# Kernel optimization log

Hardware: AMD Instinct MI355X
Metric: run time of the kernel (lower is better)

The kernel has to match this reference:

```python
import jax, jax.numpy as jnp
import numpy as np

NEG_SLOPE = 0.01  # LeakyReLU default


def gcn_conv(x, src, dst, W, b, num_nodes):
    """PyG GCNConv: x' = D^-1/2 (A+I) D^-1/2 (x W) + b, self-loops added."""
    h = x @ W
    loop = jnp.arange(num_nodes)
    s = jnp.concatenate([src, loop])
    d = jnp.concatenate([dst, loop])
    deg = jax.ops.segment_sum(jnp.ones(s.shape[0], dtype=h.dtype), d,
                              num_segments=num_nodes)
    dinv = jnp.where(deg > 0, jax.lax.rsqrt(deg), 0.0)
    norm = dinv[s] * dinv[d]              # (Ep+N,)
    out = jax.ops.segment_sum(h[s] * norm[:, None], d, num_segments=num_nodes)
    return out + b


def leaky_relu(x):
    return jnp.where(x > 0, x, NEG_SLOPE * x)


def setup_inputs() -> dict:
    key = jax.random.key(0)
    ks = jax.random.split(key, 8)
    B, V, E, Fsub, H = 16, 100000, 300000, 800000, 16
    verts = jax.random.normal(ks[0], (B, V, 3), dtype=jnp.float32)
    edges = jax.random.randint(ks[1], (E, 2), 0, V)
    faces_sub = jax.random.randint(ks[2], (Fsub, 3), 0, V + E)
    W1 = jax.random.normal(ks[3], (3, H), dtype=jnp.float32) * 0.01
    W2 = jax.random.normal(ks[4], (H, H), dtype=jnp.float32) * 0.01
    W3 = jax.random.normal(ks[5], (H, 3), dtype=jnp.float32) * 0.01
    return {"verts": verts, "edges": edges, "faces_sub": faces_sub,
            "W1": W1, "b1": jnp.zeros((H,), jnp.float32),
            "W2": W2, "b2": jnp.zeros((H,), jnp.float32),
            "W3": W3, "b3": jnp.zeros((3,), jnp.float32)}


def reference(verts, edges, faces_sub, W1, b1, W2, b2, W3, b3):
    B, V, _ = verts.shape
    E = edges.shape[0]
    N = B * V
    # pack edges across the batch (same topology per mesh, offset per mesh)
    offsets = (jnp.arange(B) * V).astype(edges.dtype)
    pe = (edges[None, :, :] + offsets[:, None, None]).reshape(B * E, 2)
    src, dst = pe[:, 0], pe[:, 1]

    x = verts.reshape(N, 3)
    h = leaky_relu(gcn_conv(x, src, dst, W1, b1, N))
    h = leaky_relu(gcn_conv(h, src, dst, W2, b2, N))
    # Dropout(0.5) is identity at inference
    offs = gcn_conv(h, src, dst, W3, b3, N)

    v = (x + offs).reshape(B, V, 3)          # offset_verts
    mid = v[:, edges].mean(axis=2)           # (B, E, 3) edge midpoints
    new_verts = jnp.concatenate([v, mid], axis=1)   # (B, V+E, 3)
    new_faces = jnp.broadcast_to(faces_sub[None], (B,) + faces_sub.shape)
    return new_verts, new_faces
```

## Files before the change

kernel.cpp:

```cpp
#include <hip/hip_runtime.h>
#include <hip/hip_bf16.h>

#define NEG_SLOPE 0.01f

typedef long long i64;
typedef __hip_bfloat16 bf16;

__device__ __forceinline__ float lrelu(float x) { return x > 0.f ? x : NEG_SLOPE * x; }
__device__ __forceinline__ float b2f(bf16 v) { return __bfloat162float(v); }
__device__ __forceinline__ float lo2f(unsigned u) { return __uint_as_float(u << 16); }
__device__ __forceinline__ float hi2f(unsigned u) { return __uint_as_float(u & 0xffff0000u); }
__device__ __forceinline__ unsigned pk2(float a, float b) {
    unsigned ua = __bfloat16_as_ushort(__float2bfloat16(a));
    unsigned ub = __bfloat16_as_ushort(__float2bfloat16(b));
    return ua | (ub << 16);
}
__device__ __forceinline__ void acc8(float* h, uint4 u) {
    h[0] += lo2f(u.x); h[1] += hi2f(u.x);
    h[2] += lo2f(u.y); h[3] += hi2f(u.y);
    h[4] += lo2f(u.z); h[5] += hi2f(u.z);
    h[6] += lo2f(u.w); h[7] += hi2f(u.w);
}

__device__ __forceinline__ void decode_bxb(int wg, int NB, int CBc, int& b, int& xb) {
    if ((CBc & 7) == 0) {
        int xcd = wg & 7, k = wg >> 3;
        int bl = k / NB;
        xb = k - bl * NB;
        b = xcd + 8 * bl;
    } else {
        b = wg / NB;
        xb = wg - b * NB;
    }
}

__global__ __launch_bounds__(256) void k_deg(const int* __restrict__ edges,
                                             int* __restrict__ indeg, int E) {
    int e = blockIdx.x * 256 + threadIdx.x;
    if (e < E) atomicAdd(&indeg[edges[2 * e + 1]], 1);
}

__global__ __launch_bounds__(256) void k_dinv(const int* __restrict__ indeg,
                                              float* __restrict__ dinv, int V) {
    int v = blockIdx.x * 256 + threadIdx.x;
    if (v < V) dinv[v] = rsqrtf((float)indeg[v] + 1.0f);
}

__global__ __launch_bounds__(256) void k_scan1(const int* __restrict__ indeg,
                                               int* __restrict__ rowptr,
                                               int* __restrict__ bsum, int V) {
    __shared__ int s[256];
    int i = blockIdx.x * 256 + threadIdx.x;
    int x = (i < V) ? indeg[i] : 0;
    s[threadIdx.x] = x;
    __syncthreads();
    for (int off = 1; off < 256; off <<= 1) {
        int t = (threadIdx.x >= (unsigned)off) ? s[threadIdx.x - off] : 0;
        __syncthreads();
        s[threadIdx.x] += t;
        __syncthreads();
    }
    if (i < V) rowptr[i] = s[threadIdx.x] - x;
    if (threadIdx.x == 255) bsum[blockIdx.x] = s[255];
}

__global__ __launch_bounds__(1024) void k_scan2(int* __restrict__ bsum, int NB) {
    __shared__ int s[1024];
    __shared__ int srun;
    if (threadIdx.x == 0) srun = 0;
    __syncthreads();
    for (int base = 0; base < NB; base += 1024) {
        int i = base + threadIdx.x;
        int x = (i < NB) ? bsum[i] : 0;
        s[threadIdx.x] = x;
        __syncthreads();
        for (int off = 1; off < 1024; off <<= 1) {
            int t = (threadIdx.x >= (unsigned)off) ? s[threadIdx.x - off] : 0;
            __syncthreads();
            s[threadIdx.x] += t;
            __syncthreads();
        }
        int run = srun;
        if (i < NB) bsum[i] = run + s[threadIdx.x] - x;
        __syncthreads();
        if (threadIdx.x == 1023) srun = run + s[1023];
        __syncthreads();
    }
}

__global__ __launch_bounds__(256) void k_scan3(int* __restrict__ rowptr,
                                               const int* __restrict__ bsum,
                                               int V, int E) {
    int i = blockIdx.x * 256 + threadIdx.x;
    if (i < V) rowptr[i] += bsum[blockIdx.x];
    if (i == 0) rowptr[V] = E;
}

__global__ __launch_bounds__(256) void k_fill(const int* __restrict__ edges,
                                              const int* __restrict__ rowptr,
                                              int* __restrict__ cur,
                                              int* __restrict__ col, int E) {
    int e = blockIdx.x * 256 + threadIdx.x;
    if (e >= E) return;
    int s = edges[2 * e], d = edges[2 * e + 1];
    int p = atomicAdd(&cur[d], 1);
    col[rowptr[d] + p] = s;
}

__global__ __launch_bounds__(256) void k_gl12(const int* __restrict__ rowptr,
                                              const int* __restrict__ col,
                                              const float* __restrict__ verts,
                                              const float* __restrict__ W1,
                                              const float* __restrict__ b1,
                                              const float* __restrict__ W2,
                                              const float* __restrict__ dinv,
                                              bf16* __restrict__ PB,
                                              float* __restrict__ Q,
                                              int b0, int V, int NB, int CBc) {
    int b, xb;
    decode_bxb(blockIdx.x, NB, CBc, b, xb);
    int v = xb * 256 + threadIdx.x;
    if (v >= V) return;
    i64 vg = (i64)(b0 + b) * V;
    i64 vb = (i64)b * V;
    float di = dinv[v];
    const float* xv = verts + (vg + v) * 3;
    float x0 = xv[0], x1 = xv[1], x2 = xv[2];
    float a0 = di * x0, a1 = di * x1, a2 = di * x2;
    float h[16];
#pragma unroll
    for (int f = 0; f < 16; ++f)
        h[f] = a0 * W1[f] + a1 * W1[16 + f] + a2 * W1[32 + f];
    int r0 = rowptr[v], r1 = rowptr[v + 1];
#pragma unroll 2
    for (int j = r0; j < r1; ++j) {
        int s = col[j];
        float ds = dinv[s];
        const float* xs = verts + (vg + s) * 3;
        float y0 = ds * xs[0], y1 = ds * xs[1], y2 = ds * xs[2];
#pragma unroll
        for (int f = 0; f < 16; ++f)
            h[f] += y0 * W1[f] + y1 * W1[16 + f] + y2 * W1[32 + f];
    }
#pragma unroll
    for (int f = 0; f < 16; ++f) h[f] = lrelu(di * h[f] + b1[f]);
    float g[16];
#pragma unroll
    for (int f = 0; f < 16; ++f) g[f] = 0.f;
#pragma unroll
    for (int k = 0; k < 16; ++k) {
        float hk = h[k];
#pragma unroll
        for (int f = 0; f < 16; ++f) g[f] += hk * W2[k * 16 + f];
    }
#pragma unroll
    for (int f = 0; f < 16; ++f) g[f] *= di;
    i64 m = vb + v;
    uint4* Pp = (uint4*)(PB + m * 16);
    Pp[0] = make_uint4(pk2(g[0], g[1]), pk2(g[2], g[3]), pk2(g[4], g[5]), pk2(g[6], g[7]));
    Pp[1] = make_uint4(pk2(g[8], g[9]), pk2(g[10], g[11]), pk2(g[12], g[13]), pk2(g[14], g[15]));
    float4* Qp = (float4*)(Q + m * 16);
#pragma unroll
    for (int q = 0; q < 4; ++q)
        Qp[q] = make_float4(g[4 * q], g[4 * q + 1], g[4 * q + 2], g[4 * q + 3]);
}

__global__ __launch_bounds__(256) void k_gl3(const int* __restrict__ rowptr,
                                             const int* __restrict__ col,
                                             const float* __restrict__ W3,
                                             const float* __restrict__ b2,
                                             const float* __restrict__ dinv,
                                             const bf16* __restrict__ Pin,
                                             const float* __restrict__ Q,
                                             float* __restrict__ R,
                                             int V, int NB, int CBc) {
    int b, xb;
    decode_bxb(blockIdx.x, NB, CBc, b, xb);
    int v = xb * 256 + threadIdx.x;
    if (v >= V) return;
    i64 vb = (i64)b * V;
    i64 m = vb + v;
    float h[16];
    const float4* Qin = (const float4*)(Q + m * 16);
#pragma unroll
    for (int q = 0; q < 4; ++q) {
        float4 t = Qin[q];
        h[4 * q] = t.x; h[4 * q + 1] = t.y; h[4 * q + 2] = t.z; h[4 * q + 3] = t.w;
    }
    const uint4* Pb = (const uint4*)(Pin + vb * 16);
    int r0 = rowptr[v], r1 = rowptr[v + 1];
    int j = r0;
    for (; j + 1 < r1; j += 2) {
        size_t u0 = (size_t)col[j] * 2, u1 = (size_t)col[j + 1] * 2;
        uint4 q0 = Pb[u0], q1 = Pb[u0 + 1];
        uint4 c0 = Pb[u1], c1 = Pb[u1 + 1];
        acc8(h, q0); acc8(h + 8, q1);
        acc8(h, c0); acc8(h + 8, c1);
    }
    if (j < r1) {
        size_t u0 = (size_t)col[j] * 2;
        uint4 q0 = Pb[u0], q1 = Pb[u0 + 1];
        acc8(h, q0); acc8(h + 8, q1);
    }
    float di = dinv[v];
    float g0 = 0.f, g1 = 0.f, g2 = 0.f;
#pragma unroll
    for (int k = 0; k < 16; ++k) {
        float hk = lrelu(di * h[k] + b2[k]);
        g0 += hk * W3[k * 3 + 0];
        g1 += hk * W3[k * 3 + 1];
        g2 += hk * W3[k * 3 + 2];
    }
    ((float4*)R)[m] = make_float4(di * g0, di * g1, di * g2, 0.f);
}

__global__ __launch_bounds__(256) void k_gvert(const int* __restrict__ rowptr,
                                               const int* __restrict__ col,
                                               const float* __restrict__ x,
                                               const float* __restrict__ b3,
                                               const float* __restrict__ dinv,
                                               const float* __restrict__ R,
                                               float* __restrict__ Vpos,
                                               float* __restrict__ out0,
                                               int b0, int V, int E, int NB, int CBc) {
    int b, xb;
    decode_bxb(blockIdx.x, NB, CBc, b, xb);
    int v = xb * 256 + threadIdx.x;
    if (v >= V) return;
    i64 vb = (i64)b * V;
    i64 m = vb + v;
    const float4* Rb = (const float4*)R + vb;
    float4 s = Rb[v];
    int r0 = rowptr[v], r1 = rowptr[v + 1];
    int j = r0;
    for (; j + 1 < r1; j += 2) {
        float4 t0 = Rb[col[j]];
        float4 t1 = Rb[col[j + 1]];
        s.x += t0.x + t1.x; s.y += t0.y + t1.y; s.z += t0.z + t1.z;
    }
    if (j < r1) {
        float4 t0 = Rb[col[j]];
        s.x += t0.x; s.y += t0.y; s.z += t0.z;
    }
    float di = dinv[v];
    int bg = b0 + b;
    i64 n = (i64)bg * V + v;
    float p0 = x[n * 3]     + di * s.x + b3[0];
    float p1 = x[n * 3 + 1] + di * s.y + b3[1];
    float p2 = x[n * 3 + 2] + di * s.z + b3[2];
    ((float4*)Vpos)[m] = make_float4(p0, p1, p2, 0.f);
    i64 o = ((i64)bg * (V + E) + v) * 3;
    __builtin_nontemporal_store(p0, out0 + o);
    __builtin_nontemporal_store(p1, out0 + o + 1);
    __builtin_nontemporal_store(p2, out0 + o + 2);
}

__global__ __launch_bounds__(256) void k_mid(const int* __restrict__ edges,
                                             const float* __restrict__ Vpos,
                                             float* __restrict__ out0,
                                             int b0, int V, int E, int NB, int CBc) {
    int b, xe;
    decode_bxb(blockIdx.x, NB, CBc, b, xe);
    int e = xe * 256 + threadIdx.x;
    if (e >= E) return;
    int s = edges[2 * e], d = edges[2 * e + 1];
    float4 ps = ((const float4*)Vpos)[(i64)b * V + s];
    float4 pd = ((const float4*)Vpos)[(i64)b * V + d];
    i64 o = ((i64)(b0 + b) * (V + E) + V + e) * 3;
    __builtin_nontemporal_store(0.5f * (ps.x + pd.x), out0 + o);
    __builtin_nontemporal_store(0.5f * (ps.y + pd.y), out0 + o + 1);
    __builtin_nontemporal_store(0.5f * (ps.z + pd.z), out0 + o + 2);
}

__global__ __launch_bounds__(256) void k_faces(const int* __restrict__ faces,
                                               float* __restrict__ out1,
                                               i64 F3, i64 faceElems) {
    i64 i = (i64)blockIdx.x * 256 + threadIdx.x;
    if (i >= F3) return;
    i64 o = (i64)blockIdx.y * F3 + i;
    if (o < faceElems) __builtin_nontemporal_store((float)faces[i], out1 + o);
}

__global__ __launch_bounds__(256) void k_l1_g(const float* __restrict__ x,
                                              const float* __restrict__ W1,
                                              const float* __restrict__ dinv,
                                              bf16* __restrict__ P, float* __restrict__ Q,
                                              int b0, int V, int H) {
    extern __shared__ float sW[];
    for (int i = threadIdx.x; i < 3 * H; i += 256) sW[i] = W1[i];
    __syncthreads();
    int v = blockIdx.x * 256 + threadIdx.x;
    if (v >= V) return;
    i64 n = (i64)(b0 + blockIdx.y) * V + v;
    i64 m = (i64)blockIdx.y * V + v;
    float di = dinv[v];
    float x0 = x[n * 3], x1 = x[n * 3 + 1], x2 = x[n * 3 + 2];
    for (int f = 0; f < H; ++f) {
        float g = di * (x0 * sW[f] + x1 * sW[H + f] + x2 * sW[2 * H + f]);
        P[m * H + f] = __float2bfloat16(g);
        Q[m * H + f] = g;
    }
}

__global__ __launch_bounds__(256) void k_scatter_g(const int* __restrict__ edges,
                                                   const bf16* __restrict__ P,
                                                   float* __restrict__ Q,
                                                   int E, int V, int H) {
    int e = blockIdx.x * 256 + threadIdx.x;
    if (e >= E) return;
    int b = blockIdx.y;
    int s = edges[2 * e], d = edges[2 * e + 1];
    for (int f = 0; f < H; ++f)
        unsafeAtomicAdd(&Q[((i64)b * V + d) * H + f], b2f(P[((i64)b * V + s) * H + f]));
}

__global__ __launch_bounds__(256) void k_l2_g(const float* __restrict__ W2,
                                              const float* __restrict__ b1,
                                              const float* __restrict__ dinv,
                                              bf16* __restrict__ P, float* __restrict__ Q,
                                              int V, int H) {
    extern __shared__ float sW[];
    float* sb = sW + H * H;
    for (int i = threadIdx.x; i < H * H; i += 256) sW[i] = W2[i];
    for (int i = threadIdx.x; i < H; i += 256) sb[i] = b1[i];
    __syncthreads();
    int v = blockIdx.x * 256 + threadIdx.x;
    if (v >= V) return;
    i64 m = (i64)blockIdx.y * V + v;
    float di = dinv[v];
    float h[64];
    for (int k = 0; k < H; ++k) h[k] = lrelu(di * Q[m * H + k] + sb[k]);
    for (int f = 0; f < H; ++f) {
        float a = 0.f;
        for (int k = 0; k < H; ++k) a += h[k] * sW[k * H + f];
        float g = di * a;
        P[m * H + f] = __float2bfloat16(g);
        Q[m * H + f] = g;
    }
}

__global__ __launch_bounds__(256) void k_l3_g(const float* __restrict__ W3,
                                              const float* __restrict__ b2,
                                              const float* __restrict__ dinv,
                                              float* __restrict__ R,
                                              const float* __restrict__ Q, int V, int H) {
    extern __shared__ float sW[];
    float* sb = sW + H * 3;
    for (int i = threadIdx.x; i < H * 3; i += 256) sW[i] = W3[i];
    for (int i = threadIdx.x; i < H; i += 256) sb[i] = b2[i];
    __syncthreads();
    int v = blockIdx.x * 256 + threadIdx.x;
    if (v >= V) return;
    i64 m = (i64)blockIdx.y * V + v;
    float di = dinv[v];
    float g0 = 0.f, g1 = 0.f, g2 = 0.f;
    for (int k = 0; k < H; ++k) {
        float h = lrelu(di * Q[m * H + k] + sb[k]);
        g0 += h * sW[k * 3]; g1 += h * sW[k * 3 + 1]; g2 += h * sW[k * 3 + 2];
    }
    ((float4*)R)[m] = make_float4(di * g0, di * g1, di * g2, 0.f);
}

extern "C" void kernel_launch(void* const* d_in, const int* in_sizes, int n_in,
                              void* d_out, int out_size, void* d_ws, size_t ws_size,
                              hipStream_t stream) {
    const float* verts = (const float*)d_in[0];
    const int*   edges = (const int*)d_in[1];
    const int*   faces = (const int*)d_in[2];
    const float* W1 = (const float*)d_in[3];
    const float* b1 = (const float*)d_in[4];
    const float* W2 = (const float*)d_in[5];
    const float* b2 = (const float*)d_in[6];
    const float* W3 = (const float*)d_in[7];
    const float* b3 = (const float*)d_in[8];

    const i64 s0 = in_sizes[0];
    const i64 E  = in_sizes[1] / 2;
    const i64 F  = in_sizes[2] / 3;
    const int H  = in_sizes[4];
    i64 B = 0;
    const i64 denomB = 3 * (E + F);
    if ((i64)out_size > s0 && denomB > 0) {
        i64 Bc = ((i64)out_size - s0) / denomB;
        if (Bc >= 1 && s0 + Bc * denomB == (i64)out_size && s0 % (3 * Bc) == 0) B = Bc;
    }
    if (B == 0) {
        i64 num = (i64)out_size - s0 - 3 * F;
        if (num > 0 && E > 0 && num % (3 * E) == 0) {
            i64 Bc = num / (3 * E);
            if (Bc >= 1 && s0 % (3 * Bc) == 0) B = Bc;
        }
    }
    if (B == 0) B = 16;
    const i64 V = s0 / (3 * B);

    const i64 Vp  = (V + 255) & ~255LL;
    const i64 NB1 = Vp >> 8;
    const size_t AUX = (size_t)Vp * 4  + (size_t)Vp * 4
                     + (size_t)(Vp + 256) * 4
                     + (size_t)(NB1 + 256) * 4
                     + (size_t)E * 4  + 1024;
    const size_t rowB = (size_t)(6 * H) + 96 + 64;
    i64 CB = B;
    while (CB > 1 && AUX + (size_t)CB * V * rowB + 8192 > ws_size) CB = (CB + 1) / 2;

    float* ws     = (float*)d_ws;
    float* dinv   = ws;
    int*   indeg  = (int*)(ws + Vp);
    int*   rowptr = indeg + Vp;
    int*   bsum   = rowptr + Vp + 256;
    int*   col    = bsum + NB1 + 256;
    char*  base   = (char*)(((size_t)(col + E) + 255) & ~(size_t)255);
    auto pad = [](size_t x) { return (x + 255) & ~(size_t)255; };

    bf16 *PB = nullptr, *Pg = nullptr;
    float *Q, *R, *Vb;
    {
        char* p = base;
        if (H == 16) {
            PB = (bf16*)p;  p += pad((size_t)CB * V * 32);
            Q  = (float*)p; p += pad((size_t)CB * V * 64);
        } else {
            Pg = (bf16*)p;  p += pad((size_t)CB * V * 2 * H);
            Q  = (float*)p; p += pad((size_t)CB * V * 4 * H);
        }
        R  = (float*)p; p += pad((size_t)CB * V * 16);
        Vb = (float*)p;
    }

    const unsigned NBv = (unsigned)((V + 255) / 256);
    const unsigned NBe = (unsigned)((E + 255) / 256);

    hipMemsetAsync(indeg, 0, V * sizeof(int), stream);
    if (NBe) k_deg<<<dim3(NBe), 256, 0, stream>>>(edges, indeg, (int)E);
    k_dinv<<<dim3(NBv), 256, 0, stream>>>(indeg, dinv, (int)V);
    k_scan1<<<dim3(NBv), 256, 0, stream>>>(indeg, rowptr, bsum, (int)V);
    k_scan2<<<dim3(1), 1024, 0, stream>>>(bsum, (int)NBv);
    k_scan3<<<dim3(NBv), 256, 0, stream>>>(rowptr, bsum, (int)V, (int)E);
    hipMemsetAsync(indeg, 0, V * sizeof(int), stream);
    if (NBe) k_fill<<<dim3(NBe), 256, 0, stream>>>(edges, rowptr, indeg, col, (int)E);

    float* out0 = (float*)d_out;
    const i64 vertElems = B * (V + E) * 3;
    float* out1 = out0 + vertElems;
    const i64 faceElems = (i64)out_size - vertElems;

    for (i64 b0 = 0; b0 < B; b0 += CB) {
        const i64 CBc = (B - b0 < CB) ? (B - b0) : CB;
        dim3 g1((unsigned)(NBv * CBc));
        dim3 g1e((unsigned)(NBe * CBc));
        if (H == 16) {
            k_gl12<<<g1, 256, 0, stream>>>(rowptr, col, verts, W1, b1, W2, dinv,
                                           PB, Q, (int)b0, (int)V, (int)NBv, (int)CBc);
            k_gl3<<<g1, 256, 0, stream>>>(rowptr, col, W3, b2, dinv, PB, Q, R,
                                          (int)V, (int)NBv, (int)CBc);
        } else {
            dim3 gn(NBv, (unsigned)CBc);
            dim3 ge(NBe, (unsigned)CBc);
            size_t sh1 = (size_t)3 * H * 4;
            size_t sh2 = ((size_t)H * H + H) * 4;
            size_t sh3 = ((size_t)H * 3 + H) * 4;
            k_l1_g<<<gn, 256, sh1, stream>>>(verts, W1, dinv, Pg, Q, (int)b0, (int)V, H);
            if (NBe) k_scatter_g<<<ge, 256, 0, stream>>>(edges, Pg, Q, (int)E, (int)V, H);
            k_l2_g<<<gn, 256, sh2, stream>>>(W2, b1, dinv, Pg, Q, (int)V, H);
            if (NBe) k_scatter_g<<<ge, 256, 0, stream>>>(edges, Pg, Q, (int)E, (int)V, H);
            k_l3_g<<<gn, 256, sh3, stream>>>(W3, b2, dinv, R, Q, (int)V, H);
        }
        k_gvert<<<g1, 256, 0, stream>>>(rowptr, col, verts, b3, dinv, R, Vb, out0,
                                        (int)b0, (int)V, (int)E, (int)NBv, (int)CBc);
        if (NBe) k_mid<<<g1e, 256, 0, stream>>>(edges, Vb, out0, (int)b0, (int)V, (int)E,
                                                (int)NBe, (int)CBc);
    }
    const i64 F3 = 3 * F;
    if (faceElems > 0 && F3 > 0)
        k_faces<<<dim3((unsigned)((F3 + 255) / 256), (unsigned)B), 256, 0, stream>>>(
            faces, out1, F3, faceElems);
}
```

Before: 534.2 us.

## Aggregate raw xyz before W1, pack rowptr pairs, vectorize faces copy

Layer 1 now sums the normalized 3-component neighbour inputs first and applies the 3x16 W1 matrix once per node, instead of multiplying by W1 for every edge. This removes most of the per-edge FLOPs in that kernel. The change also folds the dinv computation into the first scan kernel, adds an int2 row-pointer array so each node does a single load for its range, reads edges as int2 in the midpoint kernel, and adds an int4-vectorized faces conversion kernel. The cost is an extra small kernel launch for rp2 and some extra workspace.

```diff
diff --git a/kernel.cpp b/kernel.cpp
--- a/kernel.cpp
+++ b/kernel.cpp
@@ -40,18 +40,14 @@
     if (e < E) atomicAdd(&indeg[edges[2 * e + 1]], 1);
 }
 
-__global__ __launch_bounds__(256) void k_dinv(const int* __restrict__ indeg,
-                                              float* __restrict__ dinv, int V) {
-    int v = blockIdx.x * 256 + threadIdx.x;
-    if (v < V) dinv[v] = rsqrtf((float)indeg[v] + 1.0f);
-}
-
 __global__ __launch_bounds__(256) void k_scan1(const int* __restrict__ indeg,
                                                int* __restrict__ rowptr,
-                                               int* __restrict__ bsum, int V) {
+                                               int* __restrict__ bsum,
+                                               float* __restrict__ dinv, int V) {
     __shared__ int s[256];
     int i = blockIdx.x * 256 + threadIdx.x;
     int x = (i < V) ? indeg[i] : 0;
+    if (i < V) dinv[i] = rsqrtf((float)x + 1.0f);
     s[threadIdx.x] = x;
     __syncthreads();
     for (int off = 1; off < 256; off <<= 1) {
@@ -96,6 +92,12 @@
     if (i == 0) rowptr[V] = E;
 }
 
+__global__ __launch_bounds__(256) void k_rp2(const int* __restrict__ rowptr,
+                                             int2* __restrict__ rp2, int V) {
+    int v = blockIdx.x * 256 + threadIdx.x;
+    if (v < V) rp2[v] = make_int2(rowptr[v], rowptr[v + 1]);
+}
+
 __global__ __launch_bounds__(256) void k_fill(const int* __restrict__ edges,
                                               const int* __restrict__ rowptr,
                                               int* __restrict__ cur,
@@ -107,7 +109,7 @@
     col[rowptr[d] + p] = s;
 }
 
-__global__ __launch_bounds__(256) void k_gl12(const int* __restrict__ rowptr,
+__global__ __launch_bounds__(256) void k_gl12(const int2* __restrict__ rp2,
                                               const int* __restrict__ col,
                                               const float* __restrict__ verts,
                                               const float* __restrict__ W1,
@@ -125,25 +127,28 @@
     i64 vb = (i64)b * V;
     float di = dinv[v];
     const float* xv = verts + (vg + v) * 3;
-    float x0 = xv[0], x1 = xv[1], x2 = xv[2];
-    float a0 = di * x0, a1 = di * x1, a2 = di * x2;
+    float c0 = di * xv[0], c1 = di * xv[1], c2 = di * xv[2];
+    int2 r = rp2[v];
+    int j = r.x;
+    for (; j + 1 < r.y; j += 2) {
+        int s0 = col[j], s1 = col[j + 1];
+        float d0 = dinv[s0], d1 = dinv[s1];
+        const float* p0 = verts + (vg + s0) * 3;
+        const float* p1 = verts + (vg + s1) * 3;
+        c0 += d0 * p0[0] + d1 * p1[0];
+        c1 += d0 * p0[1] + d1 * p1[1];
+        c2 += d0 * p0[2] + d1 * p1[2];
+    }
+    if (j < r.y) {
+        int s0 = col[j];
+        float d0 = dinv[s0];
+        const float* p0 = verts + (vg + s0) * 3;
+        c0 += d0 * p0[0]; c1 += d0 * p0[1]; c2 += d0 * p0[2];
+    }
     float h[16];
 #pragma unroll
     for (int f = 0; f < 16; ++f)
-        h[f] = a0 * W1[f] + a1 * W1[16 + f] + a2 * W1[32 + f];
-    int r0 = rowptr[v], r1 = rowptr[v + 1];
-#pragma unroll 2
-    for (int j = r0; j < r1; ++j) {
-        int s = col[j];
-        float ds = dinv[s];
-        const float* xs = verts + (vg + s) * 3;
-        float y0 = ds * xs[0], y1 = ds * xs[1], y2 = ds * xs[2];
-#pragma unroll
-        for (int f = 0; f < 16; ++f)
-            h[f] += y0 * W1[f] + y1 * W1[16 + f] + y2 * W1[32 + f];
-    }
-#pragma unroll
-    for (int f = 0; f < 16; ++f) h[f] = lrelu(di * h[f] + b1[f]);
+        h[f] = lrelu(di * (c0 * W1[f] + c1 * W1[16 + f] + c2 * W1[32 + f]) + b1[f]);
     float g[16];
 #pragma unroll
     for (int f = 0; f < 16; ++f) g[f] = 0.f;
@@ -165,7 +170,7 @@
         Qp[q] = make_float4(g[4 * q], g[4 * q + 1], g[4 * q + 2], g[4 * q + 3]);
 }
 
-__global__ __launch_bounds__(256) void k_gl3(const int* __restrict__ rowptr,
+__global__ __launch_bounds__(256) void k_gl3(const int2* __restrict__ rp2,
                                              const int* __restrict__ col,
                                              const float* __restrict__ W3,
                                              const float* __restrict__ b2,
@@ -188,16 +193,16 @@
         h[4 * q] = t.x; h[4 * q + 1] = t.y; h[4 * q + 2] = t.z; h[4 * q + 3] = t.w;
     }
     const uint4* Pb = (const uint4*)(Pin + vb * 16);
-    int r0 = rowptr[v], r1 = rowptr[v + 1];
-    int j = r0;
-    for (; j + 1 < r1; j += 2) {
+    int2 r = rp2[v];
+    int j = r.x;
+    for (; j + 1 < r.y; j += 2) {
         size_t u0 = (size_t)col[j] * 2, u1 = (size_t)col[j + 1] * 2;
         uint4 q0 = Pb[u0], q1 = Pb[u0 + 1];
         uint4 c0 = Pb[u1], c1 = Pb[u1 + 1];
         acc8(h, q0); acc8(h + 8, q1);
         acc8(h, c0); acc8(h + 8, c1);
     }
-    if (j < r1) {
+    if (j < r.y) {
         size_t u0 = (size_t)col[j] * 2;
         uint4 q0 = Pb[u0], q1 = Pb[u0 + 1];
         acc8(h, q0); acc8(h + 8, q1);
@@ -214,7 +219,7 @@
     ((float4*)R)[m] = make_float4(di * g0, di * g1, di * g2, 0.f);
 }
 
-__global__ __launch_bounds__(256) void k_gvert(const int* __restrict__ rowptr,
+__global__ __launch_bounds__(256) void k_gvert(const int2* __restrict__ rp2,
                                                const int* __restrict__ col,
                                                const float* __restrict__ x,
                                                const float* __restrict__ b3,
@@ -231,14 +236,14 @@
     i64 m = vb + v;
     const float4* Rb = (const float4*)R + vb;
     float4 s = Rb[v];
-    int r0 = rowptr[v], r1 = rowptr[v + 1];
-    int j = r0;
-    for (; j + 1 < r1; j += 2) {
+    int2 r = rp2[v];
+    int j = r.x;
+    for (; j + 1 < r.y; j += 2) {
         float4 t0 = Rb[col[j]];
         float4 t1 = Rb[col[j + 1]];
         s.x += t0.x + t1.x; s.y += t0.y + t1.y; s.z += t0.z + t1.z;
     }
-    if (j < r1) {
+    if (j < r.y) {
         float4 t0 = Rb[col[j]];
         s.x += t0.x; s.y += t0.y; s.z += t0.z;
     }
@@ -263,9 +268,9 @@
     decode_bxb(blockIdx.x, NB, CBc, b, xe);
     int e = xe * 256 + threadIdx.x;
     if (e >= E) return;
-    int s = edges[2 * e], d = edges[2 * e + 1];
-    float4 ps = ((const float4*)Vpos)[(i64)b * V + s];
-    float4 pd = ((const float4*)Vpos)[(i64)b * V + d];
+    int2 sd = ((const int2*)edges)[e];
+    float4 ps = ((const float4*)Vpos)[(i64)b * V + sd.x];
+    float4 pd = ((const float4*)Vpos)[(i64)b * V + sd.y];
     i64 o = ((i64)(b0 + b) * (V + E) + V + e) * 3;
     __builtin_nontemporal_store(0.5f * (ps.x + pd.x), out0 + o);
     __builtin_nontemporal_store(0.5f * (ps.y + pd.y), out0 + o + 1);
@@ -279,6 +284,25 @@
     if (i >= F3) return;
     i64 o = (i64)blockIdx.y * F3 + i;
     if (o < faceElems) __builtin_nontemporal_store((float)faces[i], out1 + o);
+}
+
+__global__ __launch_bounds__(256) void k_faces4(const int4* __restrict__ faces4,
+                                                float* __restrict__ out1,
+                                                i64 Fq, i64 F3) {
+    i64 t = (i64)blockIdx.x * 256 + threadIdx.x;
+    if (t >= Fq) return;
+    int4 u = faces4[t];
+    float* p = out1 + (i64)blockIdx.y * F3 + t * 4;
+    __builtin_nontemporal_store((float)u.x, p);
+    __builtin_nontemporal_store((float)u.y, p + 1);
+    __builtin_nontemporal_store((float)u.z, p + 2);
+    __builtin_nontemporal_store((float)u.w, p + 3);
+}
+
+__global__ __launch_bounds__(256) void k_dinv_g(const int* __restrict__ indeg,
+                                                float* __restrict__ dinv, int V) {
+    int v = blockIdx.x * 256 + threadIdx.x;
+    if (v < V) dinv[v] = rsqrtf((float)indeg[v] + 1.0f);
 }
 
 __global__ __launch_bounds__(256) void k_l1_g(const float* __restrict__ x,
@@ -399,6 +423,7 @@
     const size_t AUX = (size_t)Vp * 4  + (size_t)Vp * 4
                      + (size_t)(Vp + 256) * 4
                      + (size_t)(NB1 + 256) * 4
+                     + (size_t)Vp * 8
                      + (size_t)E * 4  + 1024;
     const size_t rowB = (size_t)(6 * H) + 96 + 64;
     i64 CB = B;
@@ -409,7 +434,8 @@
     int*   indeg  = (int*)(ws + Vp);
     int*   rowptr = indeg + Vp;
     int*   bsum   = rowptr + Vp + 256;
-    int*   col    = bsum + NB1 + 256;
+    int2*  rp2    = (int2*)(bsum + NB1 + 256);
+    int*   col    = (int*)(rp2 + Vp);
     char*  base   = (char*)(((size_t)(col + E) + 255) & ~(size_t)255);
     auto pad = [](size_t x) { return (x + 255) & ~(size_t)255; };
 
@@ -433,10 +459,10 @@
 
     hipMemsetAsync(indeg, 0, V * sizeof(int), stream);
     if (NBe) k_deg<<<dim3(NBe), 256, 0, stream>>>(edges, indeg, (int)E);
-    k_dinv<<<dim3(NBv), 256, 0, stream>>>(indeg, dinv, (int)V);
-    k_scan1<<<dim3(NBv), 256, 0, stream>>>(indeg, rowptr, bsum, (int)V);
+    k_scan1<<<dim3(NBv), 256, 0, stream>>>(indeg, rowptr, bsum, dinv, (int)V);
     k_scan2<<<dim3(1), 1024, 0, stream>>>(bsum, (int)NBv);
     k_scan3<<<dim3(NBv), 256, 0, stream>>>(rowptr, bsum, (int)V, (int)E);
+    k_rp2<<<dim3(NBv), 256, 0, stream>>>(rowptr, rp2, (int)V);
     hipMemsetAsync(indeg, 0, V * sizeof(int), stream);
     if (NBe) k_fill<<<dim3(NBe), 256, 0, stream>>>(edges, rowptr, indeg, col, (int)E);
 
@@ -450,9 +476,9 @@
         dim3 g1((unsigned)(NBv * CBc));
         dim3 g1e((unsigned)(NBe * CBc));
         if (H == 16) {
-            k_gl12<<<g1, 256, 0, stream>>>(rowptr, col, verts, W1, b1, W2, dinv,
+            k_gl12<<<g1, 256, 0, stream>>>(rp2, col, verts, W1, b1, W2, dinv,
                                            PB, Q, (int)b0, (int)V, (int)NBv, (int)CBc);
-            k_gl3<<<g1, 256, 0, stream>>>(rowptr, col, W3, b2, dinv, PB, Q, R,
+            k_gl3<<<g1, 256, 0, stream>>>(rp2, col, W3, b2, dinv, PB, Q, R,
                                           (int)V, (int)NBv, (int)CBc);
         } else {
             dim3 gn(NBv, (unsigned)CBc);
@@ -466,13 +492,21 @@
             if (NBe) k_scatter_g<<<ge, 256, 0, stream>>>(edges, Pg, Q, (int)E, (int)V, H);
             k_l3_g<<<gn, 256, sh3, stream>>>(W3, b2, dinv, R, Q, (int)V, H);
         }
-        k_gvert<<<g1, 256, 0, stream>>>(rowptr, col, verts, b3, dinv, R, Vb, out0,
+        k_gvert<<<g1, 256, 0, stream>>>(rp2, col, verts, b3, dinv, R, Vb, out0,
                                         (int)b0, (int)V, (int)E, (int)NBv, (int)CBc);
         if (NBe) k_mid<<<g1e, 256, 0, stream>>>(edges, Vb, out0, (int)b0, (int)V, (int)E,
                                                 (int)NBe, (int)CBc);
     }
     const i64 F3 = 3 * F;
-    if (faceElems > 0 && F3 > 0)
-        k_faces<<<dim3((unsigned)((F3 + 255) / 256), (unsigned)B), 256, 0, stream>>>(
-            faces, out1, F3, faceElems);
-}
+    if (faceElems > 0 && F3 > 0) {
+        bool v4 = ((F3 & 3) == 0) && ((vertElems & 3) == 0) && (faceElems == B * F3);
+        if (v4) {
+            const i64 Fq = F3 >> 2;
+            k_faces4<<<dim3((unsigned)((Fq + 255) / 256), (unsigned)B), 256, 0, stream>>>(
+                (const int4*)faces, out1, Fq, F3);
+        } else {
+            k_faces<<<dim3((unsigned)((F3 + 255) / 256), (unsigned)B), 256, 0, stream>>>(
+                faces, out1, F3, faceElems);
+        }
+    }
+}
```

After: 504.0 us. 1.06x faster.
